# Optimization experiments

Hardware: AMD Instinct MI355X
Metric: run time of the kernel (lower is better)

The kernel has to match this reference:

```python
import jax, jax.numpy as jnp
import numpy as np


def setup_inputs() -> dict:
    key = jax.random.key(0)
    k1, k2, k3 = jax.random.split(key, 3)
    B, Tc, Tq, D = 8, 4096, 1024, 256
    context = jax.random.normal(k1, (B, Tc, D), dtype=jnp.float32)
    question = jax.random.normal(k2, (B, Tq, D), dtype=jnp.float32)
    w = jax.random.normal(k3, (3 * D, 1), dtype=jnp.float32) * 0.05
    return {"context": context, "question": question, "w": w}


def reference(context, question, w):
    # context: (B, Tc, D); question: (B, Tq, D); w: (3D, 1)
    D = context.shape[-1]
    w1, w2, w3 = w[:D, 0], w[D:2 * D, 0], w[2 * D:, 0]
    # Fused similarity: S[b,i,j] = w1.c_i + w2.q_j + w3.(c_i*q_j)
    # (mathematically identical to the tiled concat + linear score, but
    # avoids materializing the (B,Tc,Tq,3D) tensor)
    s_c = jnp.einsum('bid,d->bi', context, w1)              # (B, Tc)
    s_q = jnp.einsum('bjd,d->bj', question, w2)             # (B, Tq)
    s_cq = jnp.einsum('bid,bjd->bij', context * w3, question)  # (B, Tc, Tq)
    S = s_cq + s_c[:, :, None] + s_q[:, None, :]
    A = jax.nn.softmax(S, axis=-1)                           # (B, Tc, Tq)
    # C2Q attention: U[b,i] = sum_j A[b,i,j] * q_j
    U = jnp.einsum('bij,bjd->bid', A, question)              # (B, Tc, D)
    # Q2C attention: b_i = max_j A[b,i,j]; h = sum_i b_i * c_i, tiled over Tc
    b = jnp.max(A, axis=-1)                                  # (B, Tc)
    h = jnp.einsum('bi,bid->bd', b, context)                 # (B, D)
    H = jnp.broadcast_to(h[:, None, :], context.shape)       # (B, Tc, D)
    # megamerge
    G = jnp.concatenate([context, U, context * U, context * H], axis=-1)
    return G  # (B, Tc, 4D)
```

## Files before the change

### kernel.cpp

```cpp
#include <hip/hip_runtime.h>
#include <hip/hip_bf16.h>
#include <stdint.h>
#include <stddef.h>


#define NB 8
#define TC 4096
#define TQ 1024
#define DD 256
#define JT 32
#define NJT (TQ / JT)

typedef __attribute__((ext_vector_type(4)))  float  f32x4v;
typedef __attribute__((ext_vector_type(8)))  __bf16 bf16x8v;
typedef __attribute__((ext_vector_type(4)))  __bf16 bf16x4v;

#define QA_OFF   0
#define QX_OFF   (QA_OFF + NB*NJT*16*1024)
#define SQ_OFF   (QX_OFF + NB*NJT*16*1024)
#define HV_OFF   (SQ_OFF + NB*TQ*4)

__device__ __forceinline__ void async_cp16(const void* g, void* l) {
  __builtin_amdgcn_global_load_lds(
      (const __attribute__((address_space(1))) void*)g,
      (__attribute__((address_space(3))) void*)l, 16, 0, 0);
}

__global__ __launch_bounds__(256) void k_qprep(const float* __restrict__ question,
                                               const float* __restrict__ w,
                                               char* __restrict__ ws) {
  uint4* qa = (uint4*)(ws + QA_OFF);
  uint4* qx = (uint4*)(ws + QX_OFF);
  float* sq = (float*)(ws + SQ_OFF);
  __shared__ __align__(16) __bf16 T[32][264];

  int bx = blockIdx.x;
  int b = bx >> 5, it = bx & 31;
  int t = threadIdx.x;
  int j = t >> 3;
  int seg = t & 7;

  const float* qrow = question + ((size_t)(b * TQ + it * JT + j)) * DD + seg * 32;
  const float* w2 = w + DD;

  float part = 0.f;
#pragma unroll
  for (int k = 0; k < 8; ++k) {
    float4 v  = *(const float4*)(qrow + 4 * k);
    float4 wv = *(const float4*)(w2 + seg * 32 + 4 * k);
    part += v.x * wv.x + v.y * wv.y + v.z * wv.z + v.w * wv.w;
    bf16x4v pk = {(__bf16)v.x, (__bf16)v.y, (__bf16)v.z, (__bf16)v.w};
    *(bf16x4v*)&T[j][seg * 32 + 4 * k] = pk;
  }
  part += __shfl_xor(part, 1);
  part += __shfl_xor(part, 2);
  part += __shfl_xor(part, 4);
  if (seg == 0) sq[b * TQ + it * JT + j] = part;
  __syncthreads();

#pragma unroll
  for (int p = 0; p < 4; ++p) {
    int ch = t + 256 * p;
    int L = ch & 63, cc = ch >> 6;
    int jm = cc >> 3, c = cc & 7;
    int nh = L & 15, qh = L >> 4;
    uint4 v = *(const uint4*)&T[16 * jm + nh][32 * c + 8 * qh];
    qa[(size_t)(b * NJT + it) * 1024 + ch] = v;
  }
#pragma unroll
  for (int p = 0; p < 4; ++p) {
    int ch = t + 256 * p;
    int L = ch & 63, mt = ch >> 6;
    int nh = L & 15, qh = L >> 4;
    __bf16 e[8];
#pragma unroll
    for (int o = 0; o < 8; ++o) e[o] = T[8 * qh + o][16 * mt + nh];
    qx[(size_t)(b * NJT + it) * 1024 + ch] = *(const uint4*)e;
  }
}

__global__ __launch_bounds__(256, 2) void k_main(const float* __restrict__ context,
                                                 const float* __restrict__ w,
                                                 const char* __restrict__ ws,
                                                 float* __restrict__ hv,
                                                 float* __restrict__ out) {
  const uint4*  qa = (const uint4*)(ws + QA_OFF);
  const __bf16* qx = (const __bf16*)(ws + QX_OFF);
  const float*  sq = (const float*)(ws + SQ_OFF);

  __shared__ __align__(16) __bf16 qa_lds[2][8192];
  __shared__ __align__(16) __bf16 pa_lds[4][16][40];
  __shared__ __align__(16) float  sq_all[TQ];
  __shared__ __align__(16) float  red_lm[2][4][16][2];
  __shared__ __align__(16) float  rinv_lds[64];
  __shared__ __align__(16) float  bvv_lds[64];

  int bx = blockIdx.x;
  int b = bx & 7;
  int ig = bx >> 3;
  int t = threadIdx.x;
  int wv = t >> 6;
  int lane = t & 63;
  int wi = wv >> 1;
  int wj = wv & 1;
  int it0 = 2 * wi, it1 = 2 * wi + 1;
  int nh = lane & 15;
  int qh = lane >> 4;

  const uint4* qa_b = qa + (size_t)b * NJT * 1024;
  const __bf16* qx_b = qx + (size_t)b * NJT * 8192;
  const float* sqb = sq + b * TQ;

  bf16x8v cw3f0[8], cw3f1[8];
  {
    const float* crow0 = context + ((size_t)(b * TC + ig * 64 + 32 * wi + nh)) * DD;
    const float* crow1 = crow0 + 16 * DD;
    const float* w3 = w + 2 * DD;
#pragma unroll
    for (int c = 0; c < 8; ++c) {
      int d0 = 32 * c + 8 * qh;
      float4 g0 = *(const float4*)(w3 + d0);
      float4 g1 = *(const float4*)(w3 + d0 + 4);
      float4 f0 = *(const float4*)(crow0 + d0);
      float4 f1 = *(const float4*)(crow0 + d0 + 4);
      bf16x8v fr;
      fr[0] = (__bf16)(f0.x * g0.x); fr[1] = (__bf16)(f0.y * g0.y);
      fr[2] = (__bf16)(f0.z * g0.z); fr[3] = (__bf16)(f0.w * g0.w);
      fr[4] = (__bf16)(f1.x * g1.x); fr[5] = (__bf16)(f1.y * g1.y);
      fr[6] = (__bf16)(f1.z * g1.z); fr[7] = (__bf16)(f1.w * g1.w);
      cw3f0[c] = fr;
      float4 h0 = *(const float4*)(crow1 + d0);
      float4 h1 = *(const float4*)(crow1 + d0 + 4);
      bf16x8v hr;
      hr[0] = (__bf16)(h0.x * g0.x); hr[1] = (__bf16)(h0.y * g0.y);
      hr[2] = (__bf16)(h0.z * g0.z); hr[3] = (__bf16)(h0.w * g0.w);
      hr[4] = (__bf16)(h1.x * g1.x); hr[5] = (__bf16)(h1.y * g1.y);
      hr[6] = (__bf16)(h1.z * g1.z); hr[7] = (__bf16)(h1.w * g1.w);
      cw3f1[c] = hr;
    }
  }

  {
    ((float4*)sq_all)[t] = ((const float4*)sqb)[t];
    const uint4* src = qa_b;
#pragma unroll
    for (int p = 0; p < 4; ++p) {
      int cb = wv * 64 + p * 256;
      async_cp16(src + cb + lane, &qa_lds[0][(size_t)cb * 8]);
    }
  }

  f32x4v U[16];
#pragma unroll
  for (int k = 0; k < 16; ++k) U[k] = (f32x4v){0.f, 0.f, 0.f, 0.f};
  float m0_run = -1e30f, l0_run = 0.f;
  float m1_run = -1e30f, l1_run = 0.f;

  __syncthreads();

  for (int itq = 0; itq < NJT; ++itq) {
    int cur = itq & 1;

    bf16x8v bqr[4];
    {
      const __bf16* qxt = qx_b + (size_t)itq * 8192 + lane * 8;
#pragma unroll
      for (int nt = 0; nt < 4; ++nt)
        bqr[nt] = *(const bf16x8v*)(qxt + (size_t)(wv * 4 + nt) * 512);
    }

    if (itq + 1 < NJT) {
      const uint4* src = qa_b + (size_t)(itq + 1) * 1024;
#pragma unroll
      for (int p = 0; p < 4; ++p) {
        int cb = wv * 64 + p * 256;
        async_cp16(src + cb + lane, &qa_lds[cur ^ 1][(size_t)cb * 8]);
      }
    }

    f32x4v S0 = {0.f, 0.f, 0.f, 0.f}, S1 = {0.f, 0.f, 0.f, 0.f};
#pragma unroll
    for (int c = 0; c < 8; ++c) {
      bf16x8v ac = *(const bf16x8v*)&qa_lds[cur][((wj * 8 + c) * 64 + lane) * 8];
      S0 = __builtin_amdgcn_mfma_f32_16x16x32_bf16(ac, cw3f0[c], S0, 0, 0, 0);
      S1 = __builtin_amdgcn_mfma_f32_16x16x32_bf16(ac, cw3f1[c], S1, 0, 0, 0);
    }

    float4 sqv = *(const float4*)&sq_all[itq * JT + 16 * wj + 4 * qh];
    float a0 = S0[0] + sqv.x, a1 = S0[1] + sqv.y, a2 = S0[2] + sqv.z, a3 = S0[3] + sqv.w;
    float b0 = S1[0] + sqv.x, b1 = S1[1] + sqv.y, b2 = S1[2] + sqv.z, b3 = S1[3] + sqv.w;
    float e0 = __expf(a0), e1 = __expf(a1), e2 = __expf(a2), e3 = __expf(a3);
    float f0 = __expf(b0), f1 = __expf(b1), f2 = __expf(b2), f3 = __expf(b3);
    m0_run = fmaxf(m0_run, fmaxf(fmaxf(a0, a1), fmaxf(a2, a3)));
    m1_run = fmaxf(m1_run, fmaxf(fmaxf(b0, b1), fmaxf(b2, b3)));
    l0_run += (e0 + e1) + (e2 + e3);
    l1_run += (f0 + f1) + (f2 + f3);

    bf16x4v pk0 = {(__bf16)e0, (__bf16)e1, (__bf16)e2, (__bf16)e3};
    bf16x4v pk1 = {(__bf16)f0, (__bf16)f1, (__bf16)f2, (__bf16)f3};
    *(bf16x4v*)&pa_lds[it0][nh][16 * wj + 4 * qh] = pk0;
    *(bf16x4v*)&pa_lds[it1][nh][16 * wj + 4 * qh] = pk1;

    asm volatile("s_waitcnt lgkmcnt(0)\n\ts_barrier" ::: "memory");

#pragma unroll
    for (int mi = 0; mi < 4; ++mi) {
      bf16x8v af = *(const bf16x8v*)&pa_lds[mi][nh][8 * qh];
#pragma unroll
      for (int nt = 0; nt < 4; ++nt)
        U[mi * 4 + nt] = __builtin_amdgcn_mfma_f32_16x16x32_bf16(af, bqr[nt], U[mi * 4 + nt], 0, 0, 0);
    }

    __syncthreads();
  }

  float lo0 = l0_run + __shfl_xor(l0_run, 16); lo0 += __shfl_xor(lo0, 32);
  float lo1 = l1_run + __shfl_xor(l1_run, 16); lo1 += __shfl_xor(lo1, 32);
  float mo0 = fmaxf(m0_run, __shfl_xor(m0_run, 16)); mo0 = fmaxf(mo0, __shfl_xor(mo0, 32));
  float mo1 = fmaxf(m1_run, __shfl_xor(m1_run, 16)); mo1 = fmaxf(mo1, __shfl_xor(mo1, 32));
  if (lane < 16) {
    red_lm[wj][it0][nh][0] = lo0; red_lm[wj][it0][nh][1] = mo0;
    red_lm[wj][it1][nh][0] = lo1; red_lm[wj][it1][nh][1] = mo1;
  }
  __syncthreads();
  if (t < 64) {
    int it = t >> 4, n = t & 15;
    float l = red_lm[0][it][n][0] + red_lm[1][it][n][0];
    float m = fmaxf(red_lm[0][it][n][1], red_lm[1][it][n][1]);
    float ri = 1.0f / l;
    rinv_lds[t] = ri;
    bvv_lds[t] = __expf(m) * ri;
  }
  __syncthreads();

  float hacc[4] = {0.f, 0.f, 0.f, 0.f};
#pragma unroll
  for (int mi = 0; mi < 4; ++mi) {
#pragma unroll
    for (int r = 0; r < 4; ++r) {
      int rl = mi * 16 + 4 * qh + r;
      int row = ig * 64 + rl;
      float rv = rinv_lds[rl];
      float bb = bvv_lds[rl];
      const float* crow = context + ((size_t)(b * TC + row)) * DD;
      float* orow = out + ((size_t)(b * TC + row)) * (4 * DD);
#pragma unroll
      for (int nt = 0; nt < 4; ++nt) {
        int d = wv * 64 + nt * 16 + nh;
        float c = crow[d];
        float u = U[mi * 4 + nt][r] * rv;
        orow[d] = c;
        orow[DD + d] = u;
        orow[2 * DD + d] = c * u;
        hacc[nt] += bb * c;
      }
    }
  }
#pragma unroll
  for (int nt = 0; nt < 4; ++nt) {
    float h = hacc[nt] + __shfl_xor(hacc[nt], 16);
    h += __shfl_xor(h, 32);
    if (qh == 0) atomicAdd(&hv[b * DD + wv * 64 + nt * 16 + nh], h);
  }
}

__global__ __launch_bounds__(256) void k_final(const float* __restrict__ context,
                                               const char* __restrict__ ws,
                                               float* __restrict__ out) {
  const float* hv = (const float*)(ws + HV_OFF);
  int gid = blockIdx.x * 256 + threadIdx.x;
  int row = gid >> 6;
  int d = (gid & 63) * 4;
  int b = row >> 12;
  float4 c4 = ((const float4*)context)[gid];
  float4 h4 = *(const float4*)(hv + b * DD + d);
  float4 r;
  r.x = c4.x * h4.x; r.y = c4.y * h4.y; r.z = c4.z * h4.z; r.w = c4.w * h4.w;
  *(float4*)(out + (size_t)row * TQ + 3 * DD + d) = r;
}

extern "C" void kernel_launch(void* const* d_in, const int* in_sizes, int n_in,
                              void* d_out, int out_size, void* d_ws, size_t ws_size,
                              hipStream_t stream) {
  (void)in_sizes; (void)n_in; (void)out_size; (void)ws_size;
  const float* context  = (const float*)d_in[0];
  const float* question = (const float*)d_in[1];
  const float* w        = (const float*)d_in[2];
  float* out = (float*)d_out;
  char* ws = (char*)d_ws;

  k_qprep<<<NB * NJT, 256, 0, stream>>>(question, w, ws);
  hipMemsetAsync(ws + HV_OFF, 0, NB * DD * sizeof(float), stream);
  k_main<<<NB * (TC / 64), 256, 0, stream>>>(context, w, ws,
                                             (float*)(ws + HV_OFF), out);
  k_final<<<(NB * TC * DD / 4) / 256, 256, 0, stream>>>(context, ws, out);
}
```

Measured before the change: 212.6 us.

## Software-pipeline score and PV stages with double-buffered probability tiles

Double-buffers the probability tile in LDS and skews the loop so the PV MFMAs for the previous Q tile run in the same iteration as the score MFMAs and exponentials for the current tile. A prologue computes the first tile's scores and an epilogue does the last PV step. This removes one barrier per iteration and lets matrix and exp work overlap. In exchange it uses more LDS and adds register pressure that could hurt occupancy at two blocks per CU.

```diff
diff --git a/kernel.cpp b/kernel.cpp
--- a/kernel.cpp
+++ b/kernel.cpp
@@ -89,7 +89,7 @@
   const float*  sq = (const float*)(ws + SQ_OFF);
 
   __shared__ __align__(16) __bf16 qa_lds[2][8192];
-  __shared__ __align__(16) __bf16 pa_lds[4][16][40];
+  __shared__ __align__(16) __bf16 pa_lds[2][4][16][40];
   __shared__ __align__(16) float  sq_all[TQ];
   __shared__ __align__(16) float  red_lm[2][4][16][2];
   __shared__ __align__(16) float  rinv_lds[64];
@@ -158,12 +158,44 @@
 
   __syncthreads();
 
-  for (int itq = 0; itq < NJT; ++itq) {
+  {
+    {
+      const uint4* src = qa_b + 1024;
+#pragma unroll
+      for (int p = 0; p < 4; ++p) {
+        int cb = wv * 64 + p * 256;
+        async_cp16(src + cb + lane, &qa_lds[1][(size_t)cb * 8]);
+      }
+    }
+    f32x4v S0 = {0.f, 0.f, 0.f, 0.f}, S1 = {0.f, 0.f, 0.f, 0.f};
+#pragma unroll
+    for (int c = 0; c < 8; ++c) {
+      bf16x8v ac = *(const bf16x8v*)&qa_lds[0][((wj * 8 + c) * 64 + lane) * 8];
+      S0 = __builtin_amdgcn_mfma_f32_16x16x32_bf16(ac, cw3f0[c], S0, 0, 0, 0);
+      S1 = __builtin_amdgcn_mfma_f32_16x16x32_bf16(ac, cw3f1[c], S1, 0, 0, 0);
+    }
+    float4 sqv = *(const float4*)&sq_all[16 * wj + 4 * qh];
+    float a0 = S0[0] + sqv.x, a1 = S0[1] + sqv.y, a2 = S0[2] + sqv.z, a3 = S0[3] + sqv.w;
+    float b0 = S1[0] + sqv.x, b1 = S1[1] + sqv.y, b2 = S1[2] + sqv.z, b3 = S1[3] + sqv.w;
+    float e0 = __expf(a0), e1 = __expf(a1), e2 = __expf(a2), e3 = __expf(a3);
+    float f0 = __expf(b0), f1 = __expf(b1), f2 = __expf(b2), f3 = __expf(b3);
+    m0_run = fmaxf(m0_run, fmaxf(fmaxf(a0, a1), fmaxf(a2, a3)));
+    m1_run = fmaxf(m1_run, fmaxf(fmaxf(b0, b1), fmaxf(b2, b3)));
+    l0_run += (e0 + e1) + (e2 + e3);
+    l1_run += (f0 + f1) + (f2 + f3);
+    bf16x4v pk0 = {(__bf16)e0, (__bf16)e1, (__bf16)e2, (__bf16)e3};
+    bf16x4v pk1 = {(__bf16)f0, (__bf16)f1, (__bf16)f2, (__bf16)f3};
+    *(bf16x4v*)&pa_lds[0][it0][nh][16 * wj + 4 * qh] = pk0;
+    *(bf16x4v*)&pa_lds[0][it1][nh][16 * wj + 4 * qh] = pk1;
+    __syncthreads();
+  }
+
+  for (int itq = 1; itq < NJT; ++itq) {
     int cur = itq & 1;
 
     bf16x8v bqr[4];
     {
-      const __bf16* qxt = qx_b + (size_t)itq * 8192 + lane * 8;
+      const __bf16* qxt = qx_b + (size_t)(itq - 1) * 8192 + lane * 8;
 #pragma unroll
       for (int nt = 0; nt < 4; ++nt)
         bqr[nt] = *(const bf16x8v*)(qxt + (size_t)(wv * 4 + nt) * 512);
@@ -184,6 +216,14 @@
       bf16x8v ac = *(const bf16x8v*)&qa_lds[cur][((wj * 8 + c) * 64 + lane) * 8];
       S0 = __builtin_amdgcn_mfma_f32_16x16x32_bf16(ac, cw3f0[c], S0, 0, 0, 0);
       S1 = __builtin_amdgcn_mfma_f32_16x16x32_bf16(ac, cw3f1[c], S1, 0, 0, 0);
+    }
+
+#pragma unroll
+    for (int mi = 0; mi < 4; ++mi) {
+      bf16x8v af = *(const bf16x8v*)&pa_lds[cur ^ 1][mi][nh][8 * qh];
+#pragma unroll
+      for (int nt = 0; nt < 4; ++nt)
+        U[mi * 4 + nt] = __builtin_amdgcn_mfma_f32_16x16x32_bf16(af, bqr[nt], U[mi * 4 + nt], 0, 0, 0);
     }
 
     float4 sqv = *(const float4*)&sq_all[itq * JT + 16 * wj + 4 * qh];
@@ -198,20 +238,25 @@
 
     bf16x4v pk0 = {(__bf16)e0, (__bf16)e1, (__bf16)e2, (__bf16)e3};
     bf16x4v pk1 = {(__bf16)f0, (__bf16)f1, (__bf16)f2, (__bf16)f3};
-    *(bf16x4v*)&pa_lds[it0][nh][16 * wj + 4 * qh] = pk0;
-    *(bf16x4v*)&pa_lds[it1][nh][16 * wj + 4 * qh] = pk1;
-
-    asm volatile("s_waitcnt lgkmcnt(0)\n\ts_barrier" ::: "memory");
-
+    *(bf16x4v*)&pa_lds[cur][it0][nh][16 * wj + 4 * qh] = pk0;
+    *(bf16x4v*)&pa_lds[cur][it1][nh][16 * wj + 4 * qh] = pk1;
+
+    __syncthreads();
+  }
+
+  {
+    bf16x8v bqr[4];
+    const __bf16* qxt = qx_b + (size_t)(NJT - 1) * 8192 + lane * 8;
+#pragma unroll
+    for (int nt = 0; nt < 4; ++nt)
+      bqr[nt] = *(const bf16x8v*)(qxt + (size_t)(wv * 4 + nt) * 512);
 #pragma unroll
     for (int mi = 0; mi < 4; ++mi) {
-      bf16x8v af = *(const bf16x8v*)&pa_lds[mi][nh][8 * qh];
+      bf16x8v af = *(const bf16x8v*)&pa_lds[(NJT - 1) & 1][mi][nh][8 * qh];
 #pragma unroll
       for (int nt = 0; nt < 4; ++nt)
         U[mi * 4 + nt] = __builtin_amdgcn_mfma_f32_16x16x32_bf16(af, bqr[nt], U[mi * 4 + nt], 0, 0, 0);
     }
-
-    __syncthreads();
   }
 
   float lo0 = l0_run + __shfl_xor(l0_run, 16); lo0 += __shfl_xor(lo0, 32);
```

Measured after the change: 212.0 us. About the same (-0.3%).
